# Kernel tuning notes

Measured on AMD Instinct MI355X. Metric: run time of the kernel, lower is better.

## Reference

```python
import jax, jax.numpy as jnp
import numpy as np
import math

DEGREE = 3
N_FEATURES = 16
BATCH = 262144
N_POLY = math.comb(N_FEATURES + DEGREE, DEGREE)  # 969


def _poly(x, degree):
    """Polynomial features up to `degree`, matching TaylorMap._poly ordering.

    Uses the Pascal-triangle column counts: for degree block d, feature i is
    multiplied against the first comb(d-1+i, d-1) columns of the previous block.
    Loops are over fixed degree/feature counts (unrolled at trace time).
    """
    n = x.shape[-1]
    b = x.shape[0]
    blocks = [jnp.ones((b, 1), x.dtype), x]
    for d in range(2, degree + 1):
        counts = [math.comb(d - 1 + j, d - 1) for j in range(n)]  # pascal row d-1
        last = blocks[-1]
        blocks.append(
            jnp.concatenate(
                [x[:, i : i + 1] * last[:, :m] for i, m in enumerate(counts)],
                axis=-1,
            )
        )
    return jnp.concatenate(blocks, axis=-1)  # [b, comb(n+degree, degree)]


def setup_inputs() -> dict:
    key = jax.random.key(0)
    kx, kw = jax.random.split(key)
    x = jax.random.normal(kx, (BATCH, N_FEATURES), dtype=jnp.float32)
    # W initialized small so the residual map stays well-conditioned
    W = jax.random.normal(kw, (N_POLY, N_FEATURES), dtype=jnp.float32) * 0.01
    return {"x": x, "W": W}


def reference(x, W):
    """TaylorMap forward: x + poly(x) @ W."""
    return x + _poly(x, DEGREE) @ W
```

## Files before the change

kernel.cpp:

```cpp
#include <hip/hip_runtime.h>

#define NSTEP 39
#define NCOL  (NSTEP * 8)

typedef _Float16 half8   __attribute__((ext_vector_type(8)));
typedef __fp16   f16x2   __attribute__((ext_vector_type(2)));
typedef __fp16   f16x4   __attribute__((ext_vector_type(4)));
typedef __fp16   f16x8   __attribute__((ext_vector_type(8)));
typedef float    float4v __attribute__((ext_vector_type(4)));

struct Cols { short mode[NCOL]; short a[NCOL]; short b[NCOL]; short o[NCOL]; };
static constexpr Cols mk_cols() {
  Cols c{};
  int k = 0;
  for (int o = 0; o < 16; o += 4) { c.mode[k] = 1; c.o[k] = (short)o; ++k; }
  c.mode[k] = 4; ++k;
  for (int a = 0; a < 16; ++a)
    for (int o = 0; o <= a; o += 4) { c.mode[k] = 2; c.a[k] = (short)a; c.o[k] = (short)o; ++k; }
  for (int a = 0; a < 16; ++a)
    for (int b = 0; b <= a; ++b)
      for (int o = a; o < 16; o += 4) {
        c.mode[k] = 3; c.a[k] = (short)a; c.b[k] = (short)b; c.o[k] = (short)o; ++k;
      }
  for (; k < NCOL; ++k) c.mode[k] = 0;
  return c;
}
static constexpr Cols COLS = mk_cols();

__global__ void build_wfrag(const float* __restrict__ W, _Float16* __restrict__ Wp) {
  const int e = blockIdx.x * 256 + threadIdx.x;
  if (e >= NSTEP * 64) return;
  const int step = e >> 6;
  const int q    = (e >> 4) & 3;
  const int n    = e & 15;
  half8 hv;
  #pragma unroll
  for (int j = 0; j < 8; ++j) {
    const int c = step * 8 + j;
    const int mode = COLS.mode[c], a = COLS.a[c], b = COLS.b[c], o = COLS.o[c];
    float v = 0.0f;
    if (mode == 3) {
      const int i = o + q;
      if (i < 16) v = W[(153 + i * (i + 1) * (i + 2) / 6 + a * (a + 1) / 2 + b) * 16 + n];
    } else if (mode == 2) {
      const int bb = o + q;
      if (bb <= a) v = W[(17 + a * (a + 1) / 2 + bb) * 16 + n];
    } else if (mode == 1) {
      const int i = o + q;
      v = W[(1 + i) * 16 + n];
      if (i == n) v += 1.0f;
    } else if (mode == 4) {
      if (q == 0) v = W[n];
    }
    hv[j] = (_Float16)v;
  }
  *(half8*)(Wp + e * 8) = hv;
}

template<int C>
__device__ __forceinline__ float colval(const float (&xr)[16], const float (&w)[16]) {
  if constexpr (COLS.mode[C] == 3)      return (xr[COLS.a[C]] * xr[COLS.b[C]]) * w[COLS.o[C]];
  else if constexpr (COLS.mode[C] == 2) return xr[COLS.a[C]] * w[COLS.o[C]];
  else if constexpr (COLS.mode[C] == 1) return w[COLS.o[C]];
  else if constexpr (COLS.mode[C] == 4) return 1.0f;
  else                                  return 0.0f;
}

template<int Q>
__device__ __forceinline__ void setw(const float (&xr)[4][16], float (&w)[4][16]) {
  #pragma unroll
  for (int t = 0; t < 4; ++t)
    #pragma unroll
    for (int o = 0; o < 16; ++o)
      w[t][o] = xr[t][(o + Q > 15) ? 15 : (o + Q)];
}

template<int S>
__device__ __forceinline__ void steps(const _Float16* __restrict__ wfq,
                                      const float (&xr)[4][16], const float (&w)[4][16],
                                      float4v (&acc)[4]) {
  if constexpr (S < NSTEP) {
    const half8 bf = *(const half8*)(wfq + S * 512);
    #pragma unroll
    for (int t = 0; t < 4; ++t) {
      const f16x2 p01 = __builtin_amdgcn_cvt_pkrtz(colval<S * 8 + 0>(xr[t], w[t]),
                                                   colval<S * 8 + 1>(xr[t], w[t]));
      const f16x2 p23 = __builtin_amdgcn_cvt_pkrtz(colval<S * 8 + 2>(xr[t], w[t]),
                                                   colval<S * 8 + 3>(xr[t], w[t]));
      const f16x2 p45 = __builtin_amdgcn_cvt_pkrtz(colval<S * 8 + 4>(xr[t], w[t]),
                                                   colval<S * 8 + 5>(xr[t], w[t]));
      const f16x2 p67 = __builtin_amdgcn_cvt_pkrtz(colval<S * 8 + 6>(xr[t], w[t]),
                                                   colval<S * 8 + 7>(xr[t], w[t]));
      const f16x4 lo = __builtin_shufflevector(p01, p23, 0, 1, 2, 3);
      const f16x4 hi = __builtin_shufflevector(p45, p67, 0, 1, 2, 3);
      const f16x8 a8 = __builtin_shufflevector(lo, hi, 0, 1, 2, 3, 4, 5, 6, 7);
      const half8 af = __builtin_bit_cast(half8, a8);
      acc[t] = __builtin_amdgcn_mfma_f32_16x16x32_f16(af, bf, acc[t], 0, 0, 0);
    }
    steps<S + 1>(wfq, xr, w, acc);
  }
}

__global__ __launch_bounds__(256, 2)
void taylor_fwd(const float* __restrict__ X, const _Float16* __restrict__ Wp,
                float* __restrict__ O) {
  __shared__ _Float16 wfrag[NSTEP * 512];
  const int tid  = threadIdx.x;
  const int lane = tid & 63;
  const int wv   = tid >> 6;
  const int m    = lane & 15;
  const int q    = lane >> 4;

  {
    float4v* dst = (float4v*)wfrag;
    const float4v* src = (const float4v*)Wp;
    #pragma unroll
    for (int i = 0; i < 10; ++i) {
      const int idx = tid + i * 256;
      if (idx < NSTEP * 64) dst[idx] = src[idx];
    }
  }
  __syncthreads();

  const int rb = blockIdx.x * 256 + wv * 64;
  float xr[4][16];
  #pragma unroll
  for (int t = 0; t < 4; ++t) {
    const float4v* xp = (const float4v*)(X + (size_t)(rb + t * 16 + m) * 16);
    #pragma unroll
    for (int c4 = 0; c4 < 4; ++c4) {
      const float4v v = xp[c4];
      xr[t][c4 * 4 + 0] = v[0]; xr[t][c4 * 4 + 1] = v[1];
      xr[t][c4 * 4 + 2] = v[2]; xr[t][c4 * 4 + 3] = v[3];
    }
  }

  float w[4][16];
  if (q == 0)      setw<0>(xr, w);
  else if (q == 1) setw<1>(xr, w);
  else if (q == 2) setw<2>(xr, w);
  else             setw<3>(xr, w);

  float4v acc[4];
  #pragma unroll
  for (int t = 0; t < 4; ++t) acc[t] = (float4v){0.f, 0.f, 0.f, 0.f};

  const _Float16* wfq = wfrag + (q * 16 + m) * 8;
  steps<0>(wfq, xr, w, acc);

  #pragma unroll
  for (int t = 0; t < 4; ++t) {
    #pragma unroll
    for (int r = 0; r < 4; ++r) {
      const int row = rb + t * 16 + q * 4 + r;
      O[(size_t)row * 16 + m] = acc[t][r];
    }
  }
}

extern "C" void kernel_launch(void* const* d_in, const int* in_sizes, int n_in,
                              void* d_out, int out_size, void* d_ws, size_t ws_size,
                              hipStream_t stream) {
  const float* X = (const float*)d_in[0];
  const float* W = (const float*)d_in[1];
  float*       O = (float*)d_out;
  _Float16*    Wp = (_Float16*)d_ws;
  const int batch = in_sizes[0] / 16;
  const int grid  = batch / 256;

  build_wfrag<<<(NSTEP * 64 + 255) / 256, 256, 0, stream>>>(W, Wp);
  taylor_fwd<<<grid, 256, 0, stream>>>(X, Wp, O);
}
```

Baseline: 90.54 us.

## Align cubic column offsets to shrink per-lane weights and double waves per block

```diff
diff --git a/kernel.cpp b/kernel.cpp
--- a/kernel.cpp
+++ b/kernel.cpp
@@ -19,7 +19,7 @@
     for (int o = 0; o <= a; o += 4) { c.mode[k] = 2; c.a[k] = (short)a; c.o[k] = (short)o; ++k; }
   for (int a = 0; a < 16; ++a)
     for (int b = 0; b <= a; ++b)
-      for (int o = a; o < 16; o += 4) {
+      for (int o = (a & ~3); o < 16; o += 4) {
         c.mode[k] = 3; c.a[k] = (short)a; c.b[k] = (short)b; c.o[k] = (short)o; ++k;
       }
   for (; k < NCOL; ++k) c.mode[k] = 0;
@@ -41,7 +41,7 @@
     float v = 0.0f;
     if (mode == 3) {
       const int i = o + q;
-      if (i < 16) v = W[(153 + i * (i + 1) * (i + 2) / 6 + a * (a + 1) / 2 + b) * 16 + n];
+      if (i >= a) v = W[(153 + i * (i + 1) * (i + 2) / 6 + a * (a + 1) / 2 + b) * 16 + n];
     } else if (mode == 2) {
       const int bb = o + q;
       if (bb <= a) v = W[(17 + a * (a + 1) / 2 + bb) * 16 + n];
@@ -58,50 +58,50 @@
 }
 
 template<int C>
-__device__ __forceinline__ float colval(const float (&xr)[16], const float (&w)[16]) {
-  if constexpr (COLS.mode[C] == 3)      return (xr[COLS.a[C]] * xr[COLS.b[C]]) * w[COLS.o[C]];
-  else if constexpr (COLS.mode[C] == 2) return xr[COLS.a[C]] * w[COLS.o[C]];
-  else if constexpr (COLS.mode[C] == 1) return w[COLS.o[C]];
+__device__ __forceinline__ float colval(const float (&xr)[16], const float (&w4)[4]) {
+  if constexpr (COLS.mode[C] == 3)      return (xr[COLS.a[C]] * xr[COLS.b[C]]) * w4[COLS.o[C] >> 2];
+  else if constexpr (COLS.mode[C] == 2) return xr[COLS.a[C]] * w4[COLS.o[C] >> 2];
+  else if constexpr (COLS.mode[C] == 1) return w4[COLS.o[C] >> 2];
   else if constexpr (COLS.mode[C] == 4) return 1.0f;
   else                                  return 0.0f;
 }
 
 template<int Q>
-__device__ __forceinline__ void setw(const float (&xr)[4][16], float (&w)[4][16]) {
+__device__ __forceinline__ void setw4(const float (&xr)[2][16], float (&w4)[2][4]) {
   #pragma unroll
-  for (int t = 0; t < 4; ++t)
+  for (int t = 0; t < 2; ++t)
     #pragma unroll
-    for (int o = 0; o < 16; ++o)
-      w[t][o] = xr[t][(o + Q > 15) ? 15 : (o + Q)];
+    for (int j = 0; j < 4; ++j)
+      w4[t][j] = xr[t][4 * j + Q];
 }
 
 template<int S>
 __device__ __forceinline__ void steps(const _Float16* __restrict__ wfq,
-                                      const float (&xr)[4][16], const float (&w)[4][16],
-                                      float4v (&acc)[4]) {
+                                      const float (&xr)[2][16], const float (&w4)[2][4],
+                                      float4v (&acc)[2]) {
   if constexpr (S < NSTEP) {
     const half8 bf = *(const half8*)(wfq + S * 512);
     #pragma unroll
-    for (int t = 0; t < 4; ++t) {
-      const f16x2 p01 = __builtin_amdgcn_cvt_pkrtz(colval<S * 8 + 0>(xr[t], w[t]),
-                                                   colval<S * 8 + 1>(xr[t], w[t]));
-      const f16x2 p23 = __builtin_amdgcn_cvt_pkrtz(colval<S * 8 + 2>(xr[t], w[t]),
-                                                   colval<S * 8 + 3>(xr[t], w[t]));
-      const f16x2 p45 = __builtin_amdgcn_cvt_pkrtz(colval<S * 8 + 4>(xr[t], w[t]),
-                                                   colval<S * 8 + 5>(xr[t], w[t]));
-      const f16x2 p67 = __builtin_amdgcn_cvt_pkrtz(colval<S * 8 + 6>(xr[t], w[t]),
-                                                   colval<S * 8 + 7>(xr[t], w[t]));
+    for (int t = 0; t < 2; ++t) {
+      const f16x2 p01 = __builtin_amdgcn_cvt_pkrtz(colval<S * 8 + 0>(xr[t], w4[t]),
+                                                   colval<S * 8 + 1>(xr[t], w4[t]));
+      const f16x2 p23 = __builtin_amdgcn_cvt_pkrtz(colval<S * 8 + 2>(xr[t], w4[t]),
+                                                   colval<S * 8 + 3>(xr[t], w4[t]));
+      const f16x2 p45 = __builtin_amdgcn_cvt_pkrtz(colval<S * 8 + 4>(xr[t], w4[t]),
+                                                   colval<S * 8 + 5>(xr[t], w4[t]));
+      const f16x2 p67 = __builtin_amdgcn_cvt_pkrtz(colval<S * 8 + 6>(xr[t], w4[t]),
+                                                   colval<S * 8 + 7>(xr[t], w4[t]));
       const f16x4 lo = __builtin_shufflevector(p01, p23, 0, 1, 2, 3);
       const f16x4 hi = __builtin_shufflevector(p45, p67, 0, 1, 2, 3);
       const f16x8 a8 = __builtin_shufflevector(lo, hi, 0, 1, 2, 3, 4, 5, 6, 7);
       const half8 af = __builtin_bit_cast(half8, a8);
       acc[t] = __builtin_amdgcn_mfma_f32_16x16x32_f16(af, bf, acc[t], 0, 0, 0);
     }
-    steps<S + 1>(wfq, xr, w, acc);
+    steps<S + 1>(wfq, xr, w4, acc);
   }
 }
 
-__global__ __launch_bounds__(256, 2)
+__global__ __launch_bounds__(512, 6)
 void taylor_fwd(const float* __restrict__ X, const _Float16* __restrict__ Wp,
                 float* __restrict__ O) {
   __shared__ _Float16 wfrag[NSTEP * 512];
@@ -115,17 +115,17 @@
     float4v* dst = (float4v*)wfrag;
     const float4v* src = (const float4v*)Wp;
     #pragma unroll
-    for (int i = 0; i < 10; ++i) {
-      const int idx = tid + i * 256;
+    for (int i = 0; i < 5; ++i) {
+      const int idx = tid + i * 512;
       if (idx < NSTEP * 64) dst[idx] = src[idx];
     }
   }
   __syncthreads();
 
-  const int rb = blockIdx.x * 256 + wv * 64;
-  float xr[4][16];
+  const int rb = blockIdx.x * 256 + wv * 32;
+  float xr[2][16];
   #pragma unroll
-  for (int t = 0; t < 4; ++t) {
+  for (int t = 0; t < 2; ++t) {
     const float4v* xp = (const float4v*)(X + (size_t)(rb + t * 16 + m) * 16);
     #pragma unroll
     for (int c4 = 0; c4 < 4; ++c4) {
@@ -135,21 +135,21 @@
     }
   }
 
-  float w[4][16];
-  if (q == 0)      setw<0>(xr, w);
-  else if (q == 1) setw<1>(xr, w);
-  else if (q == 2) setw<2>(xr, w);
-  else             setw<3>(xr, w);
+  float w4[2][4];
+  if (q == 0)      setw4<0>(xr, w4);
+  else if (q == 1) setw4<1>(xr, w4);
+  else if (q == 2) setw4<2>(xr, w4);
+  else             setw4<3>(xr, w4);
 
-  float4v acc[4];
-  #pragma unroll
-  for (int t = 0; t < 4; ++t) acc[t] = (float4v){0.f, 0.f, 0.f, 0.f};
+  float4v acc[2];
+  acc[0] = (float4v){0.f, 0.f, 0.f, 0.f};
+  acc[1] = (float4v){0.f, 0.f, 0.f, 0.f};
 
   const _Float16* wfq = wfrag + (q * 16 + m) * 8;
-  steps<0>(wfq, xr, w, acc);
+  steps<0>(wfq, xr, w4, acc);
 
   #pragma unroll
-  for (int t = 0; t < 4; ++t) {
+  for (int t = 0; t < 2; ++t) {
     #pragma unroll
     for (int r = 0; r < 4; ++r) {
       const int row = rb + t * 16 + q * 4 + r;
@@ -169,5 +169,5 @@
   const int grid  = batch / 256;
 
   build_wfrag<<<(NSTEP * 64 + 255) / 256, 256, 0, stream>>>(W, Wp);
-  taylor_fwd<<<grid, 256, 0, stream>>>(X, Wp, O);
+  taylor_fwd<<<grid, 512, 0, stream>>>(X, Wp, O);
 }
```

New measurement: 89.94 us. No clear change (-0.7%).
